# Performance work log

Measured on AMD Instinct MI355X. Metric: run time of the kernel, lower is better.

Reference implementation:

```python
import jax, jax.numpy as jnp
import numpy as np

B, S = 2, 2048          # batch, seq_len (tokens flattened to T=B*S)
HID = 2048              # hidden_size
H = 16                  # num_heads
DN, DR, DV = 128, 64, 128   # qk_nope_head_dim, qk_rope_head_dim, v_head_dim
QKD = DN + DR           # qk_head_dim = 192
QLR, KVR = 1536, 512    # q_lora_rank, kv_lora_rank
THETA = 10000.0
EPS = 1e-6
SCALE = QKD ** -0.5


def rmsnorm(x, w):
    return x * jax.lax.rsqrt(jnp.mean(x * x, axis=-1, keepdims=True) + EPS) * w


def rope_gptj(x, pos):
    # non-neox (interleaved / GPT-J) style on partial head dim DR
    # x: [T, Hx, DR], pos: [T]
    half = DR // 2
    inv_freq = 1.0 / (THETA ** (jnp.arange(half, dtype=jnp.float32) * 2.0 / DR))
    ang = pos.astype(jnp.float32)[:, None] * inv_freq[None, :]      # [T, half]
    cos = jnp.cos(ang)[:, None, :]
    sin = jnp.sin(ang)[:, None, :]
    x1 = x[..., 0::2]
    x2 = x[..., 1::2]
    o1 = x1 * cos - x2 * sin
    o2 = x2 * cos + x1 * sin
    return jnp.stack([o1, o2], axis=-1).reshape(x.shape)


def setup_inputs() -> dict:
    key = jax.random.key(0)
    ks = jax.random.split(key, 8)
    T = B * S
    positions = jnp.tile(jnp.arange(S, dtype=jnp.int64 if jax.config.jax_enable_x64 else jnp.int32), B)
    hidden_states = jax.random.normal(ks[0], (T, HID), dtype=jnp.float32)
    s = 0.02
    Wqa = jax.random.normal(ks[1], (HID, QLR), dtype=jnp.float32) * s
    q_a_ln_w = jnp.ones((QLR,), dtype=jnp.float32)
    Wqb = jax.random.normal(ks[2], (QLR, H * QKD), dtype=jnp.float32) * s
    Wkva = jax.random.normal(ks[3], (HID, KVR + DR), dtype=jnp.float32) * s
    kv_a_ln_w = jnp.ones((KVR,), dtype=jnp.float32)
    Wkvb = jax.random.normal(ks[4], (KVR, H * (DN + DV)), dtype=jnp.float32) * s
    Wo = jax.random.normal(ks[5], (H * DV, HID), dtype=jnp.float32) * s
    return {"positions": positions, "hidden_states": hidden_states, "Wqa": Wqa,
            "q_a_ln_w": q_a_ln_w, "Wqb": Wqb, "Wkva": Wkva,
            "kv_a_ln_w": kv_a_ln_w, "Wkvb": Wkvb, "Wo": Wo}


def reference(positions, hidden_states, Wqa, q_a_ln_w, Wqb, Wkva, kv_a_ln_w, Wkvb, Wo):
    T = hidden_states.shape[0]
    # --- Q path: low-rank compression ---
    ckq = hidden_states @ Wqa                       # [T, QLR]
    q_c = rmsnorm(ckq, q_a_ln_w)
    q = (q_c @ Wqb).reshape(T, H, QKD)              # [T, H, 192]
    q_nope, q_pe = q[..., :DN], q[..., DN:]
    # --- KV path: latent compression + shared rope key ---
    kv_no_split = hidden_states @ Wkva              # [T, KVR+DR]
    kv_c, k_pe = kv_no_split[:, :KVR], kv_no_split[:, KVR:]
    kv_c_normed = rmsnorm(kv_c, kv_a_ln_w)
    kv = (kv_c_normed @ Wkvb).reshape(T, H, DN + DV)
    k_nope, v = kv[..., :DN], kv[..., DN:]
    # --- RoPE on partial dims (non-neox) ---
    q_pe = rope_gptj(q_pe, positions)               # [T, H, DR]
    k_pe = rope_gptj(k_pe[:, None, :], positions)   # [T, 1, DR]
    # --- assemble full q/k per batch ---
    qf = jnp.concatenate([q_nope, q_pe], axis=-1).reshape(B, S, H, QKD)
    kf = jnp.concatenate([k_nope, jnp.broadcast_to(k_pe, (T, H, DR))], axis=-1).reshape(B, S, H, QKD)
    vf = v.reshape(B, S, H, DV)
    # --- causal attention ---
    scores = jnp.einsum('bqhd,bkhd->bhqk', qf, kf) * SCALE
    mask = jnp.tril(jnp.ones((S, S), dtype=bool))
    scores = jnp.where(mask[None, None], scores, jnp.finfo(scores.dtype).min)
    probs = jax.nn.softmax(scores, axis=-1)
    attn = jnp.einsum('bhqk,bkhd->bqhd', probs, vf).reshape(T, H * DV)
    # --- output projection ---
    return attn @ Wo                                # [T, HID]
```

## Files before the change

### kernel.cpp

```cpp
#include <hip/hip_runtime.h>
#include <hip/hip_bf16.h>

typedef __hip_bfloat16 bf16;
typedef short bf16x8 __attribute__((ext_vector_type(8)));
typedef float f32x4 __attribute__((ext_vector_type(4)));

#define MFMA16(a, b, c) __builtin_amdgcn_mfma_f32_16x16x32_bf16((a), (b), (c), 0, 0, 0)

__device__ __forceinline__ short f2bs(float f) {
  bf16 h = __float2bfloat16(f);
  return __builtin_bit_cast(short, h);
}
__device__ __forceinline__ float bs2f(short s) {
  return __bfloat162float(__builtin_bit_cast(bf16, s));
}

__device__ __forceinline__ void gload16(const void* g, const void* l) {
  __builtin_amdgcn_global_load_lds(
      (const __attribute__((address_space(1))) unsigned int*)g,
      (__attribute__((address_space(3))) unsigned int*)l, 16, 0, 0);
}

__device__ __forceinline__ void t_cvt_core(const float* __restrict__ src,
                                           bf16* __restrict__ dst, int K, int N,
                                           int bx, int by, short Ts[64][72]) {
  const long n0 = (long)bx * 64, k0 = (long)by * 64;
  const int r = threadIdx.x >> 2, c4 = threadIdx.x & 3;
  const float* s = src + (k0 + r) * (long)N + n0 + c4 * 16;
  #pragma unroll
  for (int j = 0; j < 4; ++j) {
    float4 v = *(const float4*)(s + j * 4);
    Ts[r][c4 * 16 + j * 4 + 0] = f2bs(v.x);
    Ts[r][c4 * 16 + j * 4 + 1] = f2bs(v.y);
    Ts[r][c4 * 16 + j * 4 + 2] = f2bs(v.z);
    Ts[r][c4 * 16 + j * 4 + 3] = f2bs(v.w);
  }
  __syncthreads();
  union { uint4 v; short sh[8]; } o0, o1;
  #pragma unroll
  for (int j = 0; j < 8; ++j) o0.sh[j] = Ts[c4 * 16 + j][r];
  #pragma unroll
  for (int j = 0; j < 8; ++j) o1.sh[j] = Ts[c4 * 16 + 8 + j][r];
  *(uint4*)(dst + (n0 + r) * (long)K + k0 + c4 * 16)     = o0.v;
  *(uint4*)(dst + (n0 + r) * (long)K + k0 + c4 * 16 + 8) = o1.v;
}

__global__ __launch_bounds__(256) void prep1(
    const float* __restrict__ hs_f, bf16* __restrict__ hs_c,
    const float* __restrict__ qln_f, bf16* __restrict__ qln_c,
    const float* __restrict__ kvln_f, bf16* __restrict__ kvln_c,
    const float* __restrict__ Wqa_f, const float* __restrict__ Wkva_f,
    bf16* __restrict__ arena)
{
  __shared__ __align__(16) short Ts[64][72];
  const int bid = blockIdx.x;
  if (bid < 4097) {
    int i = bid * 256 + threadIdx.x;
    const float* s; bf16* d; int idx;
    if (i < 1048576)            { s = hs_f;   d = hs_c;   idx = i; }
    else if (i < 1048576 + 192) { s = qln_f;  d = qln_c;  idx = i - 1048576; }
    else                        { s = kvln_f; d = kvln_c; idx = i - 1048768; }
    const float4* sp = (const float4*)s;
    float4 a = sp[2 * idx], b = sp[2 * idx + 1];
    union { uint4 v; short sh[8]; } o;
    o.sh[0] = f2bs(a.x); o.sh[1] = f2bs(a.y); o.sh[2] = f2bs(a.z); o.sh[3] = f2bs(a.w);
    o.sh[4] = f2bs(b.x); o.sh[5] = f2bs(b.y); o.sh[6] = f2bs(b.z); o.sh[7] = f2bs(b.w);
    ((uint4*)d)[idx] = o.v;
  } else if (bid < 4097 + 768) {
    int l = bid - 4097;
    t_cvt_core(Wqa_f, arena, 2048, 1536, l % 24, l / 24, Ts);
  } else {
    int l = bid - 4865;
    t_cvt_core(Wkva_f, arena + (size_t)1536 * 2048, 2048, 576, l % 9, l / 9, Ts);
  }
}

__global__ __launch_bounds__(256) void prep2(
    const float* __restrict__ Wqb_f, bf16* __restrict__ wqbT,
    const float* __restrict__ Wkvb_f, bf16* __restrict__ wkvbT,
    const float* __restrict__ Wo_f, bf16* __restrict__ woT)
{
  __shared__ __align__(16) short Ts[64][72];
  const int bid = blockIdx.x;
  if (bid < 1152)      t_cvt_core(Wqb_f, wqbT, 1536, 3072, bid % 48, bid / 48, Ts);
  else if (bid < 1664) { int l = bid - 1152; t_cvt_core(Wkvb_f, wkvbT, 512, 4096, l % 64, l / 64, Ts); }
  else                 { int l = bid - 1664; t_cvt_core(Wo_f, woT, 2048, 2048, l % 32, l / 32, Ts); }
}

template<bool F32OUT>
__device__ __forceinline__ void gemm_core(
    short* As, short* Bs,
    const bf16* __restrict__ A, const bf16* __restrict__ BT, void* __restrict__ Cv,
    int N, int K, int lda, int ldb, int ldc, bf16* __restrict__ C2, int ncut,
    int nx, int nwg, int lin)
{
  const int tid = threadIdx.x, lane = tid & 63, w = tid >> 6;
  const int l15 = lane & 15, l4 = lane >> 4;
  const int wr = w >> 1, wc = w & 1;
  const int sl = (lin & 7) * (nwg >> 3) + (lin >> 3);
  const long bm = (long)(sl / nx) * 128, bn = (long)(sl % nx) * 128;
  f32x4 acc[4][4] = {};

  const int srow = tid >> 3;
  const int scs = (tid & 7) ^ (srow & 7);
  const int rsw = l15 & 7;

  for (int k0 = 0; k0 < K; k0 += 64) {
    __syncthreads();
    #pragma unroll
    for (int j = 0; j < 4; ++j) {
      const unsigned lb = __builtin_amdgcn_readfirstlane((j * 256 + w * 64) * 16);
      gload16(A + (bm + j * 32 + srow) * (long)lda + k0 + scs * 8, (char*)As + lb);
      gload16(BT + (bn + j * 32 + srow) * (long)ldb + k0 + scs * 8, (char*)Bs + lb);
    }
    __syncthreads();
    #pragma unroll
    for (int kk = 0; kk < 2; ++kk) {
      bf16x8 a[4], b[4];
      const int slot = (kk * 4 + l4) ^ rsw;
      #pragma unroll
      for (int mi = 0; mi < 4; ++mi)
        a[mi] = *(const bf16x8*)&As[(wr * 64 + mi * 16 + l15) * 64 + slot * 8];
      #pragma unroll
      for (int ni = 0; ni < 4; ++ni)
        b[ni] = *(const bf16x8*)&Bs[(wc * 64 + ni * 16 + l15) * 64 + slot * 8];
      #pragma unroll
      for (int mi = 0; mi < 4; ++mi)
        #pragma unroll
        for (int ni = 0; ni < 4; ++ni)
          acc[mi][ni] = MFMA16(a[mi], b[ni], acc[mi][ni]);
    }
  }
  #pragma unroll
  for (int mi = 0; mi < 4; ++mi)
    #pragma unroll
    for (int ni = 0; ni < 4; ++ni)
      #pragma unroll
      for (int r = 0; r < 4; ++r) {
        long row = bm + wr * 64 + mi * 16 + l4 * 4 + r;
        long col = bn + wc * 64 + ni * 16 + l15;
        float v = acc[mi][ni][r];
        if (F32OUT) {
          ((float*)Cv)[row * ldc + col] = v;
        } else if (C2 && col >= ncut) {
          C2[row * 640 + (col - ncut)] = __float2bfloat16(v);
        } else {
          ((bf16*)Cv)[row * (long)ldc + col] = __float2bfloat16(v);
        }
      }
}

template<bool F32OUT>
__global__ __launch_bounds__(256) void gemm_v4(
    const bf16* __restrict__ A, const bf16* __restrict__ BT, void* __restrict__ Cv,
    int N, int K, int lda, int ldb, int ldc, bf16* __restrict__ C2, int ncut)
{
  __shared__ __align__(16) short As[128 * 64];
  __shared__ __align__(16) short Bs[128 * 64];
  const int nx = gridDim.x, nwg = nx * gridDim.y;
  const int lin = blockIdx.y * nx + blockIdx.x;
  gemm_core<F32OUT>(As, Bs, A, BT, Cv, N, K, lda, ldb, ldc, C2, ncut, nx, nwg, lin);
}

#define TS_S 139
__global__ __launch_bounds__(256) void gemm_dual(
    const bf16* __restrict__ ckq, const bf16* __restrict__ wqbT, bf16* __restrict__ q,
    const bf16* __restrict__ kvns, const bf16* __restrict__ wkvbT,
    bf16* __restrict__ Kf, bf16* __restrict__ Vt)
{
  __shared__ __align__(16) short LDSU[128 * TS_S];
  short* As = LDSU;
  short* Bs = LDSU + 8192;
  const int bid = blockIdx.x;
  if (bid < 768) {
    gemm_core<false>(As, Bs, ckq, wqbT, q, 3072, 1536, 1536, 1536, 3072, nullptr, 0,
                     24, 768, bid);
    return;
  }
  const int lin = bid - 768;
  const int tid = threadIdx.x, lane = tid & 63, w = tid >> 6;
  const int l15 = lane & 15, l4 = lane >> 4;
  const int wr = w >> 1, wc = w & 1;
  const int sl = (lin & 7) * 128 + (lin >> 3);
  const long bm = (long)(sl / 32) * 128, bn = (long)(sl % 32) * 128;
  f32x4 acc[4][4] = {};
  const int srow = tid >> 3;
  const int scs = (tid & 7) ^ (srow & 7);
  const int rsw = l15 & 7;

  for (int k0 = 0; k0 < 512; k0 += 64) {
    __syncthreads();
    #pragma unroll
    for (int j = 0; j < 4; ++j) {
      const unsigned lb = __builtin_amdgcn_readfirstlane((j * 256 + w * 64) * 16);
      gload16(kvns + (bm + j * 32 + srow) * 640L + k0 + scs * 8, (char*)As + lb);
      gload16(wkvbT + (bn + j * 32 + srow) * 512L + k0 + scs * 8, (char*)Bs + lb);
    }
    __syncthreads();
    #pragma unroll
    for (int kk = 0; kk < 2; ++kk) {
      bf16x8 a[4], b[4];
      const int slot = (kk * 4 + l4) ^ rsw;
      #pragma unroll
      for (int mi = 0; mi < 4; ++mi)
        a[mi] = *(const bf16x8*)&As[(wr * 64 + mi * 16 + l15) * 64 + slot * 8];
      #pragma unroll
      for (int ni = 0; ni < 4; ++ni)
        b[ni] = *(const bf16x8*)&Bs[(wc * 64 + ni * 16 + l15) * 64 + slot * 8];
      #pragma unroll
      for (int mi = 0; mi < 4; ++mi)
        #pragma unroll
        for (int ni = 0; ni < 4; ++ni)
          acc[mi][ni] = MFMA16(a[mi], b[ni], acc[mi][ni]);
    }
  }

  const int h = (int)(bn >> 8);
  const int lc = (int)(bn & 255);
  const int bh = (int)(bm >> 11) * 16 + h;
  const int tsb = (int)(bm & 2047);

  __syncthreads();
  #pragma unroll
  for (int mi = 0; mi < 4; ++mi)
    #pragma unroll
    for (int ni = 0; ni < 4; ++ni)
      #pragma unroll
      for (int r = 0; r < 4; ++r)
        LDSU[(wr * 64 + mi * 16 + l4 * 4 + r) * TS_S + wc * 64 + ni * 16 + l15] =
            f2bs(acc[mi][ni][r]);
  __syncthreads();

  if (lc == 0) {
    #pragma unroll
    for (int j = 0; j < 8; ++j) {
      int u = j * 256 + tid;
      int tl = u >> 4, cs = u & 15;
      union { uint4 v; short sh[8]; } o;
      #pragma unroll
      for (int i = 0; i < 8; ++i) o.sh[i] = LDSU[tl * TS_S + cs * 8 + i];
      *(uint4*)(Kf + ((size_t)bh * 2048 + tsb + tl) * 192 +
                ((cs ^ (tl & 7)) << 3)) = o.v;
    }
  } else {
    #pragma unroll
    for (int j = 0; j < 8; ++j) {
      int u = j * 256 + tid;
      int d = u >> 4, slo = u & 15;
      int k0l = (slo >> 3) << 6;
      int cs = slo & 7;
      int tb = k0l + cs * 8;
      union { uint4 v; short sh[8]; } o;
      #pragma unroll
      for (int i = 0; i < 8; ++i) o.sh[i] = LDSU[(tb + i) * TS_S + d];
      *(uint4*)(Vt + ((size_t)(bh * 128 + d)) * 2048 + tsb + k0l +
                ((cs ^ (d & 7)) << 3)) = o.v;
    }
  }
}

template<int C>
__device__ __forceinline__ void rms_core(bf16* __restrict__ xr,
                                         const bf16* __restrict__ w, float* red)
{
  constexpr int PER = C / 256;
  const int tid = threadIdx.x;
  float v[PER];
  float ss = 0.f;
  #pragma unroll
  for (int k = 0; k < PER; ++k) {
    float f = __bfloat162float(xr[tid + k * 256]);
    v[k] = f; ss += f * f;
  }
  #pragma unroll
  for (int off = 1; off < 64; off <<= 1) ss += __shfl_xor(ss, off);
  if ((tid & 63) == 0) red[tid >> 6] = ss;
  __syncthreads();
  float tot = red[0] + red[1] + red[2] + red[3];
  float scale = rsqrtf(tot / (float)C + 1e-6f);
  #pragma unroll
  for (int k = 0; k < PER; ++k)
    xr[tid + k * 256] =
        __float2bfloat16(v[k] * scale * __bfloat162float(w[tid + k * 256]));
}

__global__ __launch_bounds__(256) void rms_dual(bf16* __restrict__ ckq,
                                                const bf16* __restrict__ qw,
                                                bf16* __restrict__ kvns,
                                                const bf16* __restrict__ kvw)
{
  __shared__ float red[4];
  const int bid = blockIdx.x;
  if (bid < 4096) rms_core<1536>(ckq + (long)bid * 1536, qw, red);
  else            rms_core<512>(kvns + (long)(bid - 4096) * 640, kvw, red);
}

__global__ __launch_bounds__(256) void prep_pe(const bf16* __restrict__ kvns,
                                               bf16* __restrict__ Kf)
{
  __shared__ short pe[64];
  const int t = blockIdx.x, tid = threadIdx.x;
  if (tid < 32) {
    int i = tid;
    float p = (float)(t & 2047);
    float freq = powf(10000.0f, -(float)i / 32.0f);
    float sn, cs;
    sincosf(p * freq, &sn, &cs);
    float y1 = __bfloat162float(kvns[(long)t * 640 + 512 + 2 * i]);
    float y2 = __bfloat162float(kvns[(long)t * 640 + 512 + 2 * i + 1]);
    pe[2 * i]     = f2bs(y1 * cs - y2 * sn);
    pe[2 * i + 1] = f2bs(y2 * cs + y1 * sn);
  }
  __syncthreads();
  if (tid < 128) {
    const int hh = tid >> 3, j = tid & 7;
    const int swz = t & 7;
    const int b = t >> 11, ts = t & 2047;
    uint4 val = *(const uint4*)&pe[(j ^ swz) * 8];
    *(uint4*)(Kf + ((size_t)(b * 16 + hh) * 2048 + ts) * 192 + (16 + j) * 8) = val;
  }
}

__global__ __launch_bounds__(256) void attn_v6(const bf16* __restrict__ q,
                                               const bf16* __restrict__ Kf,
                                               const bf16* __restrict__ Vt,
                                               bf16* __restrict__ attn)
{
  __shared__ __align__(16) short Ks[64 * 192];
  __shared__ __align__(16) short Vs[128 * 64];
  __shared__ __align__(16) short Ps[4][16 * 64];
  const float SC2 = 0.10411442245076847f;
  const int tid = threadIdx.x, lane = tid & 63, w = tid >> 6;
  const int l15 = lane & 15, l4 = lane >> 4;
  const int lin = blockIdx.x;
  const int x = lin & 7, j = lin >> 3;
  const int bh = x * 4 + (j >> 4), p = j & 15;
  const int b = bh >> 4, h = bh & 15;
  const unsigned lbase = __builtin_amdgcn_readfirstlane(w * 64 * 16);

  #pragma unroll
  for (int half = 0; half < 2; ++half) {
    const int qt = half ? (31 - p) : p;
    const long qrow0 = (long)b * 2048 + qt * 64;
    const int rowt = qt * 64 + w * 16 + l15;

    bf16x8 qf[6];
    {
      const short* qrow = (const short*)q + (qrow0 + w * 16 + l15) * 3072 + h * 192;
      #pragma unroll
      for (int kc = 0; kc < 6; ++kc)
        qf[kc] = *(const bf16x8*)(qrow + kc * 32 + l4 * 8);
    }
    {
      float pos = (float)rowt;
      #pragma unroll
      for (int kc = 4; kc < 6; ++kc)
        #pragma unroll
        for (int pr = 0; pr < 4; ++pr) {
          int i = (kc - 4) * 16 + l4 * 4 + pr;
          float freq = __expf((float)i * -0.28782313662425572f);
          float sn, cs;
          sincosf(pos * freq, &sn, &cs);
          float x1 = bs2f(qf[kc][2 * pr]), x2 = bs2f(qf[kc][2 * pr + 1]);
          qf[kc][2 * pr]     = f2bs(x1 * cs - x2 * sn);
          qf[kc][2 * pr + 1] = f2bs(x2 * cs + x1 * sn);
        }
    }
    f32x4 o[8] = {};
    float mreg = -1e30f, ls = 0.f;
    const int nch = qt + 1;

    {
      const char* ksrc = (const char*)(Kf + (long)bh * 2048 * 192);
      #pragma unroll
      for (int jj = 0; jj < 6; ++jj)
        gload16(ksrc + (jj * 256 + tid) * 16, (char*)Ks + jj * 4096 + lbase);
    }
    __syncthreads();

    for (int c = 0; c < nch; ++c) {
      const int k0 = c * 64;
      {
        #pragma unroll
        for (int jj = 0; jj < 4; ++jj) {
          int seg = jj * 256 + tid;
          const bf16* vsrc = Vt + ((long)bh * 128 + (seg >> 3)) * 2048 + k0 + (seg & 7) * 8;
          gload16(vsrc, (char*)Vs + jj * 4096 + lbase);
        }
      }
      __builtin_amdgcn_s_setprio(1);
      f32x4 s[4] = {};
      #pragma unroll
      for (int kc = 0; kc < 6; ++kc)
        #pragma unroll
        for (int kg = 0; kg < 4; ++kg) {
          int row = kg * 16 + l15;
          int slot = (kc * 4 + l4) ^ (l15 & 7);
          bf16x8 kb = *(const bf16x8*)&Ks[row * 192 + slot * 8];
          s[kg] = MFMA16(kb, qf[kc], s[kg]);
        }
      __builtin_amdgcn_s_setprio(0);

      const bool diag = (c == qt);
      float pk[16];
      #pragma unroll
      for (int kg = 0; kg < 4; ++kg)
        #pragma unroll
        for (int r = 0; r < 4; ++r) {
          float v = s[kg][r];
          if (diag && (k0 + kg * 16 + l4 * 4 + r > rowt)) v = -1e30f;
          pk[kg * 4 + r] = v;
        }
      float cm = pk[0];
      #pragma unroll
      for (int i = 1; i < 16; ++i) cm = fmaxf(cm, pk[i]);
      cm = fmaxf(cm, __shfl_xor(cm, 16));
      cm = fmaxf(cm, __shfl_xor(cm, 32));
      cm *= SC2;
      if (__ballot(cm > mreg + 12.0f)) {
        float mn = fmaxf(mreg, cm);
        float al = exp2f(mreg - mn);
        ls *= al;
        float af[4];
        #pragma unroll
        for (int r = 0; r < 4; ++r) af[r] = __shfl(al, l4 * 4 + r);
        #pragma unroll
        for (int f = 0; f < 8; ++f)
          #pragma unroll
          for (int r = 0; r < 4; ++r) o[f][r] *= af[r];
        mreg = mn;
      }
      float ps = 0.f;
      #pragma unroll
      for (int i = 0; i < 16; ++i) {
        pk[i] = exp2f(fmaf(pk[i], SC2, -mreg));
        ps += pk[i];
      }
      ps += __shfl_xor(ps, 16);
      ps += __shfl_xor(ps, 32);
      ls += ps;
      #pragma unroll
      for (int kg = 0; kg < 4; ++kg)
        #pragma unroll
        for (int pr = 0; pr < 2; ++pr) {
          int key2 = kg * 16 + l4 * 4 + pr * 2;
          int sl = (key2 >> 3) ^ (l15 & 7);
          unsigned lo = (unsigned short)f2bs(pk[kg * 4 + pr * 2]);
          unsigned hi = (unsigned short)f2bs(pk[kg * 4 + pr * 2 + 1]);
          *(unsigned*)&Ps[w][l15 * 64 + sl * 8 + (key2 & 7)] = lo | (hi << 16);
        }
      __syncthreads();

      if (c + 1 < nch) {
        const char* ksrc = (const char*)(Kf + ((long)bh * 2048 + k0 + 64) * 192);
        #pragma unroll
        for (int jj = 0; jj < 6; ++jj)
          gload16(ksrc + (jj * 256 + tid) * 16, (char*)Ks + jj * 4096 + lbase);
      }

      __builtin_amdgcn_s_setprio(1);
      #pragma unroll
      for (int ks = 0; ks < 2; ++ks) {
        int psl = (ks * 4 + l4) ^ (l15 & 7);
        bf16x8 pa = *(const bf16x8*)&Ps[w][l15 * 64 + psl * 8];
        #pragma unroll
        for (int f = 0; f < 8; ++f) {
          int vrow = f * 16 + l15;
          int vsl = (ks * 4 + l4) ^ (l15 & 7);
          bf16x8 bv = *(const bf16x8*)&Vs[vrow * 64 + vsl * 8];
          o[f] = MFMA16(pa, bv, o[f]);
        }
      }
      __builtin_amdgcn_s_setprio(0);
      __syncthreads();
    }

    #pragma unroll
    for (int r = 0; r < 4; ++r) {
      float lsr = __shfl(ls, l4 * 4 + r);
      float inv = 1.0f / lsr;
      long t = qrow0 + w * 16 + l4 * 4 + r;
      bf16* dst = attn + t * 2048 + h * 128;
      #pragma unroll
      for (int f = 0; f < 8; ++f)
        dst[f * 16 + l15] = __float2bfloat16(o[f][r] * inv);
    }
  }
}

extern "C" void kernel_launch(void* const* d_in, const int* in_sizes, int n_in,
                              void* d_out, int out_size, void* d_ws, size_t ws_size,
                              hipStream_t stream) {
  const int T = 4096;
  const float* hs_f   = (const float*)d_in[1];
  const float* Wqa_f  = (const float*)d_in[2];
  const float* qln_f  = (const float*)d_in[3];
  const float* Wqb_f  = (const float*)d_in[4];
  const float* Wkva_f = (const float*)d_in[5];
  const float* kvln_f = (const float*)d_in[6];
  const float* Wkvb_f = (const float*)d_in[7];
  const float* Wo_f   = (const float*)d_in[8];

  bf16* base = (bf16*)d_ws;
  bf16* hs_c  = base;
  bf16* woT   = base;
  bf16* ckq   = base + 8388608;
  bf16* qln_c = base + 14680064;
  bf16* kvln_c= base + 14681600;
  bf16* arena = base + 14682112;
  bf16* q     = base + 21497856;
  bf16* kvns  = base + 34080768;
  bf16* Kf    = base + 36702208;
  bf16* Vt    = base + 49285120;
  bf16* attnb = ckq;

  prep1<<<5153, 256, 0, stream>>>(hs_f, hs_c, qln_f, qln_c, kvln_f, kvln_c,
                                  Wqa_f, Wkva_f, arena);
  gemm_v4<false><<<dim3(17, 32), 256, 0, stream>>>(hs_c, arena, ckq, 2176, 2048,
                                                   2048, 2048, 1536, kvns, 1536);
  rms_dual<<<8192, 256, 0, stream>>>(ckq, qln_c, kvns, kvln_c);
  prep_pe<<<T, 256, 0, stream>>>(kvns, Kf);
  prep2<<<2688, 256, 0, stream>>>(Wqb_f, arena, Wkvb_f, arena + 4718592, Wo_f, woT);
  gemm_dual<<<1792, 256, 0, stream>>>(ckq, arena, q, kvns, arena + 4718592, Kf, Vt);
  attn_v6<<<512, 256, 0, stream>>>(q, Kf, Vt, attnb);
  gemm_v4<true><<<dim3(16, 32), 256, 0, stream>>>(attnb, woT, d_out, 2048, 2048,
                                                  2048, 2048, 2048, nullptr, 0);
}
```

Measured before the change: 289.3 us.

## Merge prep kernels, fuse RMS with k_pe RoPE, double-buffer K in attention

Combines the two weight-conversion kernels into a single launch and fuses the k_pe RoPE scatter into the kv RMSNorm kernel, cutting two kernel launches and their tail gaps. The workspace layout is redone so all weights have their own regions. In attention, K tiles are double-buffered in LDS and the next tile's prefetch is issued at the top of the loop, overlapping the load with the QK and softmax work. Doubling the K buffer raises LDS use per block, which may lower occupancy.

```diff
diff --git a/kernel.cpp b/kernel.cpp
--- a/kernel.cpp
+++ b/kernel.cpp
@@ -45,12 +45,15 @@
   *(uint4*)(dst + (n0 + r) * (long)K + k0 + c4 * 16 + 8) = o1.v;
 }
 
-__global__ __launch_bounds__(256) void prep1(
+__global__ __launch_bounds__(256) void prep_all(
     const float* __restrict__ hs_f, bf16* __restrict__ hs_c,
     const float* __restrict__ qln_f, bf16* __restrict__ qln_c,
     const float* __restrict__ kvln_f, bf16* __restrict__ kvln_c,
-    const float* __restrict__ Wqa_f, const float* __restrict__ Wkva_f,
-    bf16* __restrict__ arena)
+    const float* __restrict__ Wqa_f, bf16* __restrict__ wqaT,
+    const float* __restrict__ Wkva_f, bf16* __restrict__ wkvaT,
+    const float* __restrict__ Wqb_f, bf16* __restrict__ wqbT,
+    const float* __restrict__ Wkvb_f, bf16* __restrict__ wkvbT,
+    const float* __restrict__ Wo_f, bf16* __restrict__ woT)
 {
   __shared__ __align__(16) short Ts[64][72];
   const int bid = blockIdx.x;
@@ -66,25 +69,17 @@
     o.sh[0] = f2bs(a.x); o.sh[1] = f2bs(a.y); o.sh[2] = f2bs(a.z); o.sh[3] = f2bs(a.w);
     o.sh[4] = f2bs(b.x); o.sh[5] = f2bs(b.y); o.sh[6] = f2bs(b.z); o.sh[7] = f2bs(b.w);
     ((uint4*)d)[idx] = o.v;
-  } else if (bid < 4097 + 768) {
-    int l = bid - 4097;
-    t_cvt_core(Wqa_f, arena, 2048, 1536, l % 24, l / 24, Ts);
+  } else if (bid < 4865) {
+    int l = bid - 4097;  t_cvt_core(Wqa_f, wqaT, 2048, 1536, l % 24, l / 24, Ts);
+  } else if (bid < 5153) {
+    int l = bid - 4865;  t_cvt_core(Wkva_f, wkvaT, 2048, 576, l % 9, l / 9, Ts);
+  } else if (bid < 6305) {
+    int l = bid - 5153;  t_cvt_core(Wqb_f, wqbT, 1536, 3072, l % 48, l / 48, Ts);
+  } else if (bid < 6817) {
+    int l = bid - 6305;  t_cvt_core(Wkvb_f, wkvbT, 512, 4096, l % 64, l / 64, Ts);
   } else {
-    int l = bid - 4865;
-    t_cvt_core(Wkva_f, arena + (size_t)1536 * 2048, 2048, 576, l % 9, l / 9, Ts);
-  }
-}
-
-__global__ __launch_bounds__(256) void prep2(
-    const float* __restrict__ Wqb_f, bf16* __restrict__ wqbT,
-    const float* __restrict__ Wkvb_f, bf16* __restrict__ wkvbT,
-    const float* __restrict__ Wo_f, bf16* __restrict__ woT)
-{
-  __shared__ __align__(16) short Ts[64][72];
-  const int bid = blockIdx.x;
-  if (bid < 1152)      t_cvt_core(Wqb_f, wqbT, 1536, 3072, bid % 48, bid / 48, Ts);
-  else if (bid < 1664) { int l = bid - 1152; t_cvt_core(Wkvb_f, wkvbT, 512, 4096, l % 64, l / 64, Ts); }
-  else                 { int l = bid - 1664; t_cvt_core(Wo_f, woT, 2048, 2048, l % 32, l / 32, Ts); }
+    int l = bid - 6817;  t_cvt_core(Wo_f, woT, 2048, 2048, l % 32, l / 32, Ts);
+  }
 }
 
 template<bool F32OUT>
@@ -284,22 +279,21 @@
         __float2bfloat16(v[k] * scale * __bfloat162float(w[tid + k * 256]));
 }
 
-__global__ __launch_bounds__(256) void rms_dual(bf16* __restrict__ ckq,
-                                                const bf16* __restrict__ qw,
-                                                bf16* __restrict__ kvns,
-                                                const bf16* __restrict__ kvw)
+__global__ __launch_bounds__(256) void rms_pe_dual(bf16* __restrict__ ckq,
+                                                   const bf16* __restrict__ qw,
+                                                   bf16* __restrict__ kvns,
+                                                   const bf16* __restrict__ kvw,
+                                                   bf16* __restrict__ Kf)
 {
   __shared__ float red[4];
-  const int bid = blockIdx.x;
-  if (bid < 4096) rms_core<1536>(ckq + (long)bid * 1536, qw, red);
-  else            rms_core<512>(kvns + (long)(bid - 4096) * 640, kvw, red);
-}
-
-__global__ __launch_bounds__(256) void prep_pe(const bf16* __restrict__ kvns,
-                                               bf16* __restrict__ Kf)
-{
   __shared__ short pe[64];
-  const int t = blockIdx.x, tid = threadIdx.x;
+  const int bid = blockIdx.x, tid = threadIdx.x;
+  if (bid < 4096) {
+    rms_core<1536>(ckq + (long)bid * 1536, qw, red);
+    return;
+  }
+  const int t = bid - 4096;
+  rms_core<512>(kvns + (long)t * 640, kvw, red);
   if (tid < 32) {
     int i = tid;
     float p = (float)(t & 2047);
@@ -321,12 +315,12 @@
   }
 }
 
-__global__ __launch_bounds__(256) void attn_v6(const bf16* __restrict__ q,
+__global__ __launch_bounds__(256) void attn_v7(const bf16* __restrict__ q,
                                                const bf16* __restrict__ Kf,
                                                const bf16* __restrict__ Vt,
                                                bf16* __restrict__ attn)
 {
-  __shared__ __align__(16) short Ks[64 * 192];
+  __shared__ __align__(16) short Ks[2 * 64 * 192];
   __shared__ __align__(16) short Vs[128 * 64];
   __shared__ __align__(16) short Ps[4][16 * 64];
   const float SC2 = 0.10411442245076847f;
@@ -380,6 +374,14 @@
 
     for (int c = 0; c < nch; ++c) {
       const int k0 = c * 64;
+      const int cb = (c & 1) * 24576;
+      if (c + 1 < nch) {
+        const char* ksrc = (const char*)(Kf + ((long)bh * 2048 + k0 + 64) * 192);
+        const int nb = ((c + 1) & 1) * 24576;
+        #pragma unroll
+        for (int jj = 0; jj < 6; ++jj)
+          gload16(ksrc + (jj * 256 + tid) * 16, (char*)Ks + nb + jj * 4096 + lbase);
+      }
       {
         #pragma unroll
         for (int jj = 0; jj < 4; ++jj) {
@@ -396,7 +398,7 @@
         for (int kg = 0; kg < 4; ++kg) {
           int row = kg * 16 + l15;
           int slot = (kc * 4 + l4) ^ (l15 & 7);
-          bf16x8 kb = *(const bf16x8*)&Ks[row * 192 + slot * 8];
+          bf16x8 kb = *(const bf16x8*)((const char*)Ks + cb + (row * 192 + slot * 8) * 2);
           s[kg] = MFMA16(kb, qf[kc], s[kg]);
         }
       __builtin_amdgcn_s_setprio(0);
@@ -451,13 +453,6 @@
         }
       __syncthreads();
 
-      if (c + 1 < nch) {
-        const char* ksrc = (const char*)(Kf + ((long)bh * 2048 + k0 + 64) * 192);
-        #pragma unroll
-        for (int jj = 0; jj < 6; ++jj)
-          gload16(ksrc + (jj * 256 + tid) * 16, (char*)Ks + jj * 4096 + lbase);
-      }
-
       __builtin_amdgcn_s_setprio(1);
       #pragma unroll
       for (int ks = 0; ks < 2; ++ks) {
@@ -491,7 +486,6 @@
 extern "C" void kernel_launch(void* const* d_in, const int* in_sizes, int n_in,
                               void* d_out, int out_size, void* d_ws, size_t ws_size,
                               hipStream_t stream) {
-  const int T = 4096;
   const float* hs_f   = (const float*)d_in[1];
   const float* Wqa_f  = (const float*)d_in[2];
   const float* qln_f  = (const float*)d_in[3];
@@ -503,26 +497,28 @@
 
   bf16* base = (bf16*)d_ws;
   bf16* hs_c  = base;
-  bf16* woT   = base;
-  bf16* ckq   = base + 8388608;
-  bf16* qln_c = base + 14680064;
-  bf16* kvln_c= base + 14681600;
-  bf16* arena = base + 14682112;
-  bf16* q     = base + 21497856;
-  bf16* kvns  = base + 34080768;
-  bf16* Kf    = base + 36702208;
-  bf16* Vt    = base + 49285120;
-  bf16* attnb = ckq;
-
-  prep1<<<5153, 256, 0, stream>>>(hs_f, hs_c, qln_f, qln_c, kvln_f, kvln_c,
-                                  Wqa_f, Wkva_f, arena);
-  gemm_v4<false><<<dim3(17, 32), 256, 0, stream>>>(hs_c, arena, ckq, 2176, 2048,
+  bf16* wqaT  = base + 8388608;
+  bf16* wkvaT = base + 11534336;
+  bf16* q     = base;
+  bf16* ckq   = base + 12713984;
+  bf16* qln_c = base + 19005440;
+  bf16* kvln_c= base + 19006976;
+  bf16* attnb = base + 12713984;
+  bf16* wqbT  = base + 21102592;
+  bf16* wkvbT = base + 25821184;
+  bf16* woT   = base + 27918336;
+  bf16* kvns  = base + 32112640;
+  bf16* Kf    = base + 34734080;
+  bf16* Vt    = base + 47316992;
+
+  prep_all<<<7841, 256, 0, stream>>>(hs_f, hs_c, qln_f, qln_c, kvln_f, kvln_c,
+                                     Wqa_f, wqaT, Wkva_f, wkvaT,
+                                     Wqb_f, wqbT, Wkvb_f, wkvbT, Wo_f, woT);
+  gemm_v4<false><<<dim3(17, 32), 256, 0, stream>>>(hs_c, wqaT, ckq, 2176, 2048,
                                                    2048, 2048, 1536, kvns, 1536);
-  rms_dual<<<8192, 256, 0, stream>>>(ckq, qln_c, kvns, kvln_c);
-  prep_pe<<<T, 256, 0, stream>>>(kvns, Kf);
-  prep2<<<2688, 256, 0, stream>>>(Wqb_f, arena, Wkvb_f, arena + 4718592, Wo_f, woT);
-  gemm_dual<<<1792, 256, 0, stream>>>(ckq, arena, q, kvns, arena + 4718592, Kf, Vt);
-  attn_v6<<<512, 256, 0, stream>>>(q, Kf, Vt, attnb);
+  rms_pe_dual<<<8192, 256, 0, stream>>>(ckq, qln_c, kvns, kvln_c, Kf);
+  gemm_dual<<<1792, 256, 0, stream>>>(ckq, wqbT, q, kvns, wkvbT, Kf, Vt);
+  attn_v7<<<512, 256, 0, stream>>>(q, Kf, Vt, attnb);
   gemm_v4<true><<<dim3(16, 32), 256, 0, stream>>>(attnb, woT, d_out, 2048, 2048,
                                                   2048, 2048, 2048, nullptr, 0);
 }
```

After: 283.0 us. 2.2% less time.
